# Kernel optimization log

Hardware: AMD Instinct MI355X
Metric: run time of the kernel (lower is better)

Reference implementation:

```python
import jax, jax.numpy as jnp
import numpy as np

H, NH, HD, KV, GS, L, F, V = 2048, 32, 64, 8, 4, 4, 8192, 32000
ROPE_BASE = 500000.0
EPS = 1e-5
WSCALE = 0.02


def setup_inputs() -> dict:
    key = jax.random.key(0)
    ks = jax.random.split(key, 12)
    B, S = 1, 2048
    return {
        "input_ids": jax.random.randint(ks[0], (B, S), 0, V),
        "embed": jax.random.normal(ks[1], (V, H), jnp.float32) * WSCALE,
        "ln1": jnp.ones((L, H), jnp.float32),
        "Wq": jax.random.normal(ks[2], (L, H, H), jnp.float32) * WSCALE,
        "Wk": jax.random.normal(ks[3], (L, KV * HD, H), jnp.float32) * WSCALE,
        "Wv": jax.random.normal(ks[4], (L, KV * HD, H), jnp.float32) * WSCALE,
        "Wo": jax.random.normal(ks[5], (L, H, H), jnp.float32) * WSCALE,
        "ln2": jnp.ones((L, H), jnp.float32),
        "Wg": jax.random.normal(ks[6], (L, F, H), jnp.float32) * WSCALE,
        "Wu": jax.random.normal(ks[7], (L, F, H), jnp.float32) * WSCALE,
        "Wd": jax.random.normal(ks[8], (L, H, F), jnp.float32) * WSCALE,
        "final_ln": jnp.ones((H,), jnp.float32),
    }


def _rms_norm(x, w):
    return x * jax.lax.rsqrt(jnp.mean(x * x, axis=-1, keepdims=True) + EPS) * w


def reference(input_ids, embed, ln1, Wq, Wk, Wv, Wo, ln2, Wg, Wu, Wd, final_ln):
    B, S = input_ids.shape
    h = embed[input_ids]                                   # [B,S,H]

    # RoPE tables (position_offset=0, prompt phase)
    dim_half = HD // 2
    inv_freq = 1.0 / (ROPE_BASE ** (jnp.arange(dim_half, dtype=jnp.float32) / dim_half))
    ang = jnp.arange(S, dtype=jnp.float32)[:, None] * inv_freq  # [S,dim_half]
    sin = jnp.sin(ang)[None, :, None, :]
    cos = jnp.cos(ang)[None, :, None, :]

    def rope(x):  # x: [B,S,heads,HD], halves layout as in source
        xe, xo = x[..., :dim_half], x[..., dim_half:2 * dim_half]
        return jnp.concatenate([xe * cos - xo * sin, xo * cos + xe * sin], axis=-1)

    causal = jnp.triu(jnp.ones((S, S), bool), k=1)          # [S,S]
    scale = 1.0 / (HD ** 0.5)

    for i in range(L):
        hn = _rms_norm(h, ln1[i])
        q = (hn @ Wq[i].T).reshape(B, S, NH, HD)
        k = (hn @ Wk[i].T).reshape(B, S, KV, HD)
        v = (hn @ Wv[i].T).reshape(B, S, KV, HD)
        q, k = rope(q), rope(k)
        ke = jnp.repeat(k, GS, axis=2)                      # GQA expand -> [B,S,NH,HD]
        ve = jnp.repeat(v, GS, axis=2)
        scores = jnp.einsum('bqhd,bkhd->bhqk', q, ke) * scale
        scores = jnp.where(causal[None, None], -jnp.inf, scores)
        attn = jax.nn.softmax(scores, axis=-1)
        out = jnp.einsum('bhqk,bkhd->bqhd', attn, ve).reshape(B, S, H)
        h = h + out @ Wo[i].T
        hn = _rms_norm(h, ln2[i])
        h = h + (jax.nn.silu(hn @ Wg[i].T) * (hn @ Wu[i].T)) @ Wd[i].T

    h = _rms_norm(h, final_ln)
    logits = h @ embed.T                                    # tied lm_head
    return logits
```

## Files before the change

### kernel.cpp

```cpp
#include <hip/hip_runtime.h>
#include <math.h>

#define HDIM 2048
#define SEQ 2048
#define NHEADS 32
#define KVH 8
#define HEADD 64
#define FDIM 8192
#define NLAYERS 4
#define VOCAB 32000

typedef __attribute__((ext_vector_type(4))) float f32x4;
typedef __attribute__((ext_vector_type(8))) short bf16x8;

__device__ __forceinline__ unsigned short f2b(float f) {
    unsigned int u = __float_as_uint(f);
    u += 0x7fff + ((u >> 16) & 1);
    return (unsigned short)(u >> 16);
}

__device__ __forceinline__ int xcd_swz(int bid, int nwg) {
    int xcd = bid & 7, lin = bid >> 3;
    int q = nwg >> 3, r = nwg & 7;
    return (xcd < r ? xcd * (q + 1) : r * (q + 1) + (xcd - r) * q) + lin;
}

#define GLL(gp, lp) __builtin_amdgcn_global_load_lds( \
    (const __attribute__((address_space(1))) void*)(gp), \
    (__attribute__((address_space(3))) void*)(lp), 16, 0, 0)

__device__ __forceinline__ void bar() {
    asm volatile("" ::: "memory");
    __builtin_amdgcn_s_barrier();
    asm volatile("" ::: "memory");
}

__global__ __launch_bounds__(256) void k_f2b(const float* __restrict__ src,
                                             unsigned short* __restrict__ dst, long n) {
    const long stride = (long)gridDim.x * 256 * 8;
    for (long i = ((long)blockIdx.x * 256 + threadIdx.x) * 8; i < n; i += stride) {
        float4 a = *(const float4*)(src + i);
        float4 b = *(const float4*)(src + i + 4);
        alignas(16) unsigned short t[8] = {f2b(a.x), f2b(a.y), f2b(a.z), f2b(a.w),
                                           f2b(b.x), f2b(b.y), f2b(b.z), f2b(b.w)};
        *(uint4*)(dst + i) = *(const uint4*)t;
    }
}

__global__ __launch_bounds__(256) void k_f2b_qkv(const float* __restrict__ Wq,
                                                 const float* __restrict__ Wk,
                                                 const float* __restrict__ Wv,
                                                 unsigned short* __restrict__ dst) {
    const long total = (long)NLAYERS * 3072 * 256;
    const long stride = (long)gridDim.x * 256;
    for (long u = (long)blockIdx.x * 256 + threadIdx.x; u < total; u += stride) {
        long l = u / (3072 * 256);
        long rem = u - l * (3072 * 256);
        long row = rem >> 8, cv = rem & 255;
        const float* src;
        if (row < 2048)      src = Wq + ((l * 2048 + row) << 11) + (cv << 3);
        else if (row < 2560) src = Wk + ((l * 512 + row - 2048) << 11) + (cv << 3);
        else                 src = Wv + ((l * 512 + row - 2560) << 11) + (cv << 3);
        float4 a = *(const float4*)src;
        float4 b = *(const float4*)(src + 4);
        alignas(16) unsigned short t[8] = {f2b(a.x), f2b(a.y), f2b(a.z), f2b(a.w),
                                           f2b(b.x), f2b(b.y), f2b(b.z), f2b(b.w)};
        *(uint4*)(dst + (u << 3)) = *(const uint4*)t;
    }
}

__global__ __launch_bounds__(256) void k_f2b_gu(const float* __restrict__ Wg,
                                                const float* __restrict__ Wu,
                                                unsigned short* __restrict__ dst) {
    const long total = (long)NLAYERS * 16384 * 256;
    const long stride = (long)gridDim.x * 256;
    for (long u = (long)blockIdx.x * 256 + threadIdx.x; u < total; u += stride) {
        long l = u / (16384 * 256);
        long rem = u - l * (16384 * 256);
        long row = rem >> 8, cv = rem & 255;
        long f = row >> 1;
        const float* src = ((row & 1) ? Wu : Wg) + ((l * FDIM + f) << 11) + (cv << 3);
        float4 a = *(const float4*)src;
        float4 b = *(const float4*)(src + 4);
        alignas(16) unsigned short t[8] = {f2b(a.x), f2b(a.y), f2b(a.z), f2b(a.w),
                                           f2b(b.x), f2b(b.y), f2b(b.z), f2b(b.w)};
        *(uint4*)(dst + (u << 3)) = *(const uint4*)t;
    }
}

template <int MODE, int K, int LDA, int LDB>
__global__ __launch_bounds__(512) void k_gemm256(const unsigned short* __restrict__ A,
                                                 const unsigned short* __restrict__ B,
                                                 float* __restrict__ C,
                                                 unsigned short* __restrict__ Cg,
                                                 int ldc, int mtiles, int nt,
                                                 long cstride) {
    constexpr int nK = K / 64;
    static_assert(nK >= 4 && (nK & 1) == 0, "nK must be even >= 4");
    __shared__ unsigned short As[2][2][128 * 64];
    __shared__ unsigned short Bs[2][2][128 * 64];
    const int tid  = threadIdx.x;
    const int lane = tid & 63;
    const int w    = tid >> 6;
    const int wm   = w >> 2, wn = w & 3;
    const int swz  = xcd_swz(blockIdx.x, gridDim.x);
    const int kslice = swz / nt;
    const int tile   = swz - kslice * nt;
    const int bm   = (tile % mtiles) * 256, bn = (tile / mtiles) * 256;
    const int r16  = lane & 15;
    const int l4   = lane >> 4;
    const int sw   = r16 & 7;

    const int srow = lane >> 3;
    const int scol = ((lane & 7) ^ srow) * 8;
    const unsigned short* Abase = A + (size_t)kslice * K
                                + (size_t)(bm + w * 16 + srow) * LDA + scol;
    const unsigned short* Bbase = B + (size_t)kslice * K
                                + (size_t)(bn + w * 16 + srow) * LDB + scol;

#define STG_A(bb, hh, kk) do { \
    GLL(Abase + (size_t)(hh) * 128 * LDA + (kk),       &As[(bb)][(hh)][(w * 16) * 64]); \
    GLL(Abase + (size_t)((hh) * 128 + 8) * LDA + (kk), &As[(bb)][(hh)][(w * 16 + 8) * 64]); \
} while (0)
#define STG_B(bb, hh, kk) do { \
    GLL(Bbase + (size_t)(hh) * 128 * LDB + (kk),       &Bs[(bb)][(hh)][(w * 16) * 64]); \
    GLL(Bbase + (size_t)((hh) * 128 + 8) * LDB + (kk), &Bs[(bb)][(hh)][(w * 16 + 8) * 64]); \
} while (0)

    f32x4 acc[8][4] = {};
    const int cb0 = ((0 + l4) ^ sw) * 8;
    const int cb1 = ((4 + l4) ^ sw) * 8;

    STG_A(0, 0, 0); STG_A(0, 1, 0); STG_B(0, 0, 0); STG_B(0, 1, 0);
    STG_B(1, 0, 64); STG_B(1, 1, 64); STG_A(1, 0, 64);
    asm volatile("s_waitcnt vmcnt(6)" ::: "memory");
    bar();

#define BLOAD(b) do { \
    const unsigned short* _Bh = Bs[b][wn >> 1]; \
    _Pragma("unroll") \
    for (int _n = 0; _n < 4; _n++) { \
        bq[_n][0] = *(const bf16x8*)&_Bh[((wn & 1) * 64 + _n * 16 + r16) * 64 + cb0]; \
        bq[_n][1] = *(const bf16x8*)&_Bh[((wn & 1) * 64 + _n * 16 + r16) * 64 + cb1]; \
    } \
} while (0)

#define PHASE(b, p, EXTRA, TAIL) do { \
    constexpr int _m0 = 2 * (p), _m1 = _m0 + 1; \
    const unsigned short* _Ah = As[b][_m0 >> 2]; \
    bf16x8 _a00 = *(const bf16x8*)&_Ah[(wm * 16 + (_m0 & 3) * 32 + r16) * 64 + cb0]; \
    bf16x8 _a01 = *(const bf16x8*)&_Ah[(wm * 16 + (_m0 & 3) * 32 + r16) * 64 + cb1]; \
    bf16x8 _a10 = *(const bf16x8*)&_Ah[(wm * 16 + (_m1 & 3) * 32 + r16) * 64 + cb0]; \
    bf16x8 _a11 = *(const bf16x8*)&_Ah[(wm * 16 + (_m1 & 3) * 32 + r16) * 64 + cb1]; \
    EXTRA; \
    bar(); \
    asm volatile("s_waitcnt lgkmcnt(0)" ::: "memory"); \
    __builtin_amdgcn_sched_barrier(0); \
    __builtin_amdgcn_s_setprio(1); \
    _Pragma("unroll") \
    for (int _n = 0; _n < 4; _n++) { \
        acc[_m0][_n] = __builtin_amdgcn_mfma_f32_16x16x32_bf16(_a00, bq[_n][0], acc[_m0][_n], 0, 0, 0); \
        acc[_m0][_n] = __builtin_amdgcn_mfma_f32_16x16x32_bf16(_a01, bq[_n][1], acc[_m0][_n], 0, 0, 0); \
    } \
    _Pragma("unroll") \
    for (int _n = 0; _n < 4; _n++) { \
        acc[_m1][_n] = __builtin_amdgcn_mfma_f32_16x16x32_bf16(_a10, bq[_n][0], acc[_m1][_n], 0, 0, 0); \
        acc[_m1][_n] = __builtin_amdgcn_mfma_f32_16x16x32_bf16(_a11, bq[_n][1], acc[_m1][_n], 0, 0, 0); \
    } \
    __builtin_amdgcn_s_setprio(0); \
    TAIL; \
    bar(); \
} while (0)

#define TILE_STEADY(b, t) do { \
    bf16x8 bq[4][2]; \
    PHASE(b, 0, { BLOAD(b); STG_A((b) ^ 1, 1, ((t) + 1) * 64); }, ); \
    PHASE(b, 1, STG_B(b, 0, ((t) + 2) * 64), ); \
    PHASE(b, 2, STG_B(b, 1, ((t) + 2) * 64), ); \
    PHASE(b, 3, STG_A(b, 0, ((t) + 2) * 64), \
          asm volatile("s_waitcnt vmcnt(6)" ::: "memory")); \
} while (0)

#define TILE_2NDLAST(b, t) do { \
    bf16x8 bq[4][2]; \
    PHASE(b, 0, { BLOAD(b); STG_A((b) ^ 1, 1, ((t) + 1) * 64); }, ); \
    PHASE(b, 1, , ); \
    PHASE(b, 2, , ); \
    PHASE(b, 3, , asm volatile("s_waitcnt vmcnt(0)" ::: "memory")); \
} while (0)

#define TILE_LAST(b) do { \
    bf16x8 bq[4][2]; \
    PHASE(b, 0, BLOAD(b), ); \
    PHASE(b, 1, , ); \
    PHASE(b, 2, , ); \
    PHASE(b, 3, , ); \
} while (0)

    for (int t = 0; t < nK - 2; t += 2) {
        TILE_STEADY(0, t);
        TILE_STEADY(1, t + 1);
    }
    TILE_2NDLAST(0, nK - 2);
    TILE_LAST(1);

#undef TILE_STEADY
#undef TILE_2NDLAST
#undef TILE_LAST
#undef PHASE
#undef BLOAD
#undef STG_A
#undef STG_B

    if (MODE == 0) C += (size_t)kslice * cstride;
    const int r0 = l4 * 4;
#pragma unroll
    for (int m = 0; m < 8; m++)
#pragma unroll
        for (int n = 0; n < 4; n++)
#pragma unroll
            for (int j = 0; j < 4; j++) {
                int row = bm + wm * 16 + m * 32 + r0 + j;
                int col = bn + wn * 64 + n * 16 + r16;
                if (MODE == 0) {
                    C[(size_t)row * ldc + col] = acc[m][n][j];
                } else {
                    float v0 = acc[m][n][j];
                    float v1 = __shfl_xor(v0, 1, 64);
                    if (!(r16 & 1)) {
                        float val = v0 / (1.f + __expf(-v0)) * v1;
                        Cg[(size_t)row * ldc + (col >> 1)] = f2b(val);
                    }
                }
            }
}

__global__ __launch_bounds__(256) void k_radd4(float* __restrict__ h,
                                               const float* __restrict__ P, long n4) {
    const long n = n4 * 4;
    const long stride = (long)gridDim.x * 256;
    for (long i = (long)blockIdx.x * 256 + threadIdx.x; i < n4; i += stride) {
        float4 a = ((const float4*)P)[i];
        float4 b = ((const float4*)(P + n))[i];
        float4 c = ((const float4*)(P + 2 * n))[i];
        float4 d = ((const float4*)(P + 3 * n))[i];
        float4 hh = ((float4*)h)[i];
        hh.x += a.x + b.x + c.x + d.x;
        hh.y += a.y + b.y + c.y + d.y;
        hh.z += a.z + b.z + c.z + d.z;
        hh.w += a.w + b.w + c.w + d.w;
        ((float4*)h)[i] = hh;
    }
}

template <bool ACCUM>
__global__ __launch_bounds__(256) void k_gemm_bf(const unsigned short* __restrict__ A,
                                                 const unsigned short* __restrict__ B,
                                                 float* __restrict__ C,
                                                 int K, int lda, int ldb, int ldc,
                                                 int mtiles) {
    __shared__ unsigned short As[128 * 32];
    __shared__ unsigned short Bs[128 * 32];
    const int tid  = threadIdx.x;
    const int lane = tid & 63;
    const int w    = tid >> 6;
    const int wm   = w >> 1, wn = w & 1;
    const int bid  = xcd_swz(blockIdx.x, gridDim.x);
    const int bm   = (bid % mtiles) * 128, bn = (bid / mtiles) * 128;
    const int r16  = lane & 15;
    const int l4   = lane >> 4;

    const unsigned short* Ag = A + (size_t)(bm + w * 32 + (lane >> 2)) * lda + (lane & 3) * 8;
    const unsigned short* Bg = B + (size_t)(bn + w * 32 + (lane >> 2)) * ldb + (lane & 3) * 8;
    unsigned short* Al = As + w * 1024;
    unsigned short* Bl = Bs + w * 1024;

    f32x4 acc[4][4] = {};

    for (int k0 = 0; k0 < K; k0 += 32) {
        GLL(Ag + k0,                    Al);
        GLL(Ag + k0 + (size_t)16 * lda, Al + 512);
        GLL(Bg + k0,                    Bl);
        GLL(Bg + k0 + (size_t)16 * ldb, Bl + 512);
        __syncthreads();

        bf16x8 af[4], bf[4];
#pragma unroll
        for (int m = 0; m < 4; m++) af[m] = *(const bf16x8*)&As[(wm * 64 + m * 16 + r16) * 32 + l4 * 8];
#pragma unroll
        for (int n = 0; n < 4; n++) bf[n] = *(const bf16x8*)&Bs[(wn * 64 + n * 16 + r16) * 32 + l4 * 8];
#pragma unroll
        for (int m = 0; m < 4; m++)
#pragma unroll
            for (int n = 0; n < 4; n++)
                acc[m][n] = __builtin_amdgcn_mfma_f32_16x16x32_bf16(af[m], bf[n], acc[m][n], 0, 0, 0);
        __syncthreads();
    }

    const int r0 = l4 * 4;
#pragma unroll
    for (int m = 0; m < 4; m++)
#pragma unroll
        for (int n = 0; n < 4; n++)
#pragma unroll
            for (int j = 0; j < 4; j++) {
                int row = bm + wm * 64 + m * 16 + r0 + j;
                int col = bn + wn * 64 + n * 16 + r16;
                size_t idx = (size_t)row * ldc + col;
                if (ACCUM) C[idx] += acc[m][n][j];
                else       C[idx] = acc[m][n][j];
            }
}

template <bool ACCUM>
__global__ __launch_bounds__(256) void k_gemm(const float* __restrict__ A,
                                              const float* __restrict__ B,
                                              float* __restrict__ C,
                                              int K, int lda, int ldb, int ldc) {
    __shared__ unsigned short As[128][40];
    __shared__ unsigned short Bs[128][40];
    const int tid  = threadIdx.x;
    const int lane = tid & 63;
    const int wid  = tid >> 6;
    const int wm   = wid >> 1, wn = wid & 1;
    const int bm   = blockIdx.y * 128, bn = blockIdx.x * 128;
    const int arow = tid >> 1, ahalf = tid & 1;
    const float* Ab = A + (size_t)(bm + arow) * lda + ahalf * 16;
    const float* Bb = B + (size_t)(bn + arow) * ldb + ahalf * 16;
    const int r16 = lane & 15;
    const int kk  = (lane >> 4) * 8;

    f32x4 acc[4][4] = {};

    for (int k0 = 0; k0 < K; k0 += 32) {
        alignas(16) unsigned short ta[16], tb[16];
#pragma unroll
        for (int i = 0; i < 4; i++) {
            float4 av = *(const float4*)(Ab + k0 + i * 4);
            float4 bv = *(const float4*)(Bb + k0 + i * 4);
            ta[i*4+0] = f2b(av.x); ta[i*4+1] = f2b(av.y);
            ta[i*4+2] = f2b(av.z); ta[i*4+3] = f2b(av.w);
            tb[i*4+0] = f2b(bv.x); tb[i*4+1] = f2b(bv.y);
            tb[i*4+2] = f2b(bv.z); tb[i*4+3] = f2b(bv.w);
        }
        __syncthreads();
        *(uint4*)&As[arow][ahalf*16]     = *(const uint4*)&ta[0];
        *(uint4*)&As[arow][ahalf*16 + 8] = *(const uint4*)&ta[8];
        *(uint4*)&Bs[arow][ahalf*16]     = *(const uint4*)&tb[0];
        *(uint4*)&Bs[arow][ahalf*16 + 8] = *(const uint4*)&tb[8];
        __syncthreads();

        bf16x8 af[4], bf[4];
#pragma unroll
        for (int m = 0; m < 4; m++) af[m] = *(const bf16x8*)&As[wm*64 + m*16 + r16][kk];
#pragma unroll
        for (int n = 0; n < 4; n++) bf[n] = *(const bf16x8*)&Bs[wn*64 + n*16 + r16][kk];
#pragma unroll
        for (int m = 0; m < 4; m++)
#pragma unroll
            for (int n = 0; n < 4; n++)
                acc[m][n] = __builtin_amdgcn_mfma_f32_16x16x32_bf16(af[m], bf[n], acc[m][n], 0, 0, 0);
    }

    const int r0 = (lane >> 4) * 4;
#pragma unroll
    for (int m = 0; m < 4; m++)
#pragma unroll
        for (int n = 0; n < 4; n++)
#pragma unroll
            for (int j = 0; j < 4; j++) {
                int row = bm + wm*64 + m*16 + r0 + j;
                int col = bn + wn*64 + n*16 + r16;
                size_t idx = (size_t)row * ldc + col;
                if (ACCUM) C[idx] += acc[m][n][j];
                else       C[idx] = acc[m][n][j];
            }
}

__global__ __launch_bounds__(256) void k_gather(const int* __restrict__ ids,
                                                const float* __restrict__ embed,
                                                float* __restrict__ h) {
    const int s = blockIdx.x, tid = threadIdx.x;
    const int row = ids[s];
    const float4* src = (const float4*)(embed + (size_t)row * HDIM);
    float4* dst = (float4*)(h + (size_t)s * HDIM);
    dst[tid]       = src[tid];
    dst[tid + 256] = src[tid + 256];
}

__device__ __forceinline__ float rms_scale(float4 a, float4 b, int tid) {
    float sum = a.x*a.x + a.y*a.y + a.z*a.z + a.w*a.w
              + b.x*b.x + b.y*b.y + b.z*b.z + b.w*b.w;
#pragma unroll
    for (int off = 32; off; off >>= 1) sum += __shfl_xor(sum, off, 64);
    __shared__ float red[4];
    if ((tid & 63) == 0) red[tid >> 6] = sum;
    __syncthreads();
    float tot = red[0] + red[1] + red[2] + red[3];
    return rsqrtf(tot * (1.0f / HDIM) + 1e-5f);
}

__global__ __launch_bounds__(256) void k_rmsnorm_bf(unsigned short* __restrict__ out,
                                                    const float* __restrict__ in,
                                                    const float* __restrict__ w) {
    const int s = blockIdx.x, tid = threadIdx.x;
    const float4* x = (const float4*)(in + (size_t)s * HDIM);
    float4 a = x[tid*2], b = x[tid*2+1];
    float r = rms_scale(a, b, tid);
    const float4* wv = (const float4*)w;
    float4 wa = wv[tid*2], wb = wv[tid*2+1];
    alignas(16) unsigned short t[8];
    t[0] = f2b(a.x*r*wa.x); t[1] = f2b(a.y*r*wa.y);
    t[2] = f2b(a.z*r*wa.z); t[3] = f2b(a.w*r*wa.w);
    t[4] = f2b(b.x*r*wb.x); t[5] = f2b(b.y*r*wb.y);
    t[6] = f2b(b.z*r*wb.z); t[7] = f2b(b.w*r*wb.w);
    *(uint4*)(out + (size_t)s * HDIM + tid * 8) = *(const uint4*)t;
}

__global__ __launch_bounds__(256) void k_rmsnorm_f32(float* __restrict__ out,
                                                     const float* __restrict__ in,
                                                     const float* __restrict__ w) {
    const int s = blockIdx.x, tid = threadIdx.x;
    const float4* x = (const float4*)(in + (size_t)s * HDIM);
    float4 a = x[tid*2], b = x[tid*2+1];
    float r = rms_scale(a, b, tid);
    const float4* wv = (const float4*)w;
    float4 wa = wv[tid*2], wb = wv[tid*2+1];
    float4* o = (float4*)(out + (size_t)s * HDIM);
    float4 oa, ob;
    oa.x = a.x*r*wa.x; oa.y = a.y*r*wa.y; oa.z = a.z*r*wa.z; oa.w = a.w*r*wa.w;
    ob.x = b.x*r*wb.x; ob.y = b.y*r*wb.y; ob.z = b.z*r*wb.z; ob.w = b.w*r*wb.w;
    o[tid*2] = oa; o[tid*2+1] = ob;
}

template <bool TWO>
__global__ __launch_bounds__(256) void k_ropeq(const float* __restrict__ P0,
                                               const float* __restrict__ P1,
                                               unsigned short* __restrict__ q_bf) {
    const int s = blockIdx.x, tid = threadIdx.x;
    for (int idx = tid; idx < 1024; idx += 256) {
        int hh = idx >> 5, j = idx & 31;
        float invf = exp2f(-(float)j * (18.931568569324174f / 32.0f));
        float ang = (float)s * invf;
        float sn, cs;
        __sincosf(ang, &sn, &cs);
        size_t off = (size_t)s * 3072 + hh * 64 + j;
        float xe = P0[off]      + (TWO ? P1[off]      : 0.f);
        float xo = P0[off + 32] + (TWO ? P1[off + 32] : 0.f);
        unsigned short* o = q_bf + (size_t)s * HDIM + hh * 64 + j;
        o[0]  = f2b((xe * cs - xo * sn) * 0.125f);
        o[32] = f2b((xo * cs + xe * sn) * 0.125f);
    }
}

template <bool TWO>
__global__ __launch_bounds__(256) void k_prep_kv(const float* __restrict__ P0,
                                                 const float* __restrict__ P1,
                                                 unsigned short* __restrict__ kbf,
                                                 unsigned short* __restrict__ vtb) {
    const int s0 = blockIdx.x * 64, tid = threadIdx.x;
    for (int i = tid; i < 64 * 256; i += 256) {
        int r = i >> 8, idx = i & 255;
        int kvh = idx >> 5, j = idx & 31;
        int s = s0 + r;
        float invf = exp2f(-(float)j * (18.931568569324174f / 32.0f));
        float ang = (float)s * invf;
        float sn, cs;
        __sincosf(ang, &sn, &cs);
        size_t off = (size_t)s * 3072 + 2048 + kvh * 64 + j;
        float xe = P0[off]      + (TWO ? P1[off]      : 0.f);
        float xo = P0[off + 32] + (TWO ? P1[off + 32] : 0.f);
        unsigned short* o = kbf + ((size_t)kvh * SEQ + s) * 64 + j;
        o[0]  = f2b(xe * cs - xo * sn);
        o[32] = f2b(xo * cs + xe * sn);
    }
    __shared__ float Ls[64][65];
    for (int kvh = 0; kvh < KVH; kvh++) {
        __syncthreads();
        {
            int r = tid >> 2, c0 = (tid & 3) * 16;
            size_t off = (size_t)(s0 + r) * 3072 + 2560 + kvh * 64 + c0;
#pragma unroll
            for (int i = 0; i < 16; i += 4) {
                float4 x = *(const float4*)(P0 + off + i);
                if (TWO) {
                    float4 y = *(const float4*)(P1 + off + i);
                    x.x += y.x; x.y += y.y; x.z += y.z; x.w += y.w;
                }
                Ls[r][c0+i] = x.x; Ls[r][c0+i+1] = x.y;
                Ls[r][c0+i+2] = x.z; Ls[r][c0+i+3] = x.w;
            }
        }
        __syncthreads();
        {
            int d = tid >> 2, k0 = (tid & 3) * 16;
            alignas(16) unsigned short tmp[16];
#pragma unroll
            for (int i = 0; i < 16; i++) tmp[i] = f2b(Ls[k0 + i][d]);
            unsigned short* dst = vtb + ((size_t)kvh * 64 + d) * SEQ + s0 + k0;
            *(uint4*)dst       = *(const uint4*)tmp;
            *(uint4*)(dst + 8) = *(const uint4*)(tmp + 8);
        }
    }
}

__global__ __launch_bounds__(256) void k_attn2(const unsigned short* __restrict__ q_bf,
                                               const unsigned short* __restrict__ kbf,
                                               const unsigned short* __restrict__ vtb,
                                               unsigned short* __restrict__ aob) {
    const int hh  = blockIdx.y;
    const int qt  = gridDim.x - 1 - blockIdx.x;
    const int qb  = qt * 64;
    const int kvh = hh >> 2;
    const int tid = threadIdx.x, w = tid >> 6, lane = tid & 63;
    const int r16 = lane & 15;
    const int l4  = lane >> 4;

    __shared__ unsigned short Ks[64][72];
    __shared__ unsigned short Vs[64][72];
    __shared__ unsigned short Ps[64][72];

    bf16x8 qf[2];
    {
        const unsigned short* qrow = q_bf + (size_t)(qb + w*16 + r16) * HDIM + hh * 64;
        qf[0] = *(const bf16x8*)(qrow + l4 * 8);
        qf[1] = *(const bf16x8*)(qrow + 32 + l4 * 8);
    }

    float m[4] = {-1e30f, -1e30f, -1e30f, -1e30f};
    float l[4] = {0.f, 0.f, 0.f, 0.f};
    f32x4 out[4] = {};

    for (int t = 0; t <= qt; t++) {
        __syncthreads();
        {
            int r = tid >> 2, c0 = (tid & 3) * 16;
            const unsigned short* ksrc = kbf + ((size_t)kvh * SEQ + t*64 + r) * 64 + c0;
            *(uint4*)&Ks[r][c0]     = *(const uint4*)ksrc;
            *(uint4*)&Ks[r][c0 + 8] = *(const uint4*)(ksrc + 8);
            const unsigned short* vsrc = vtb + ((size_t)kvh * 64 + r) * SEQ + t*64 + c0;
            *(uint4*)&Vs[r][c0]     = *(const uint4*)vsrc;
            *(uint4*)&Vs[r][c0 + 8] = *(const uint4*)(vsrc + 8);
        }
        __syncthreads();

        f32x4 s[4] = {};
#pragma unroll
        for (int ks = 0; ks < 2; ks++)
#pragma unroll
            for (int n = 0; n < 4; n++) {
                bf16x8 kf = *(const bf16x8*)&Ks[n*16 + r16][ks*32 + l4*8];
                s[n] = __builtin_amdgcn_mfma_f32_16x16x32_bf16(qf[ks], kf, s[n], 0, 0, 0);
            }

        if (t == qt) {
#pragma unroll
            for (int n = 0; n < 4; n++)
#pragma unroll
                for (int j = 0; j < 4; j++) {
                    int qrow = w*16 + l4*4 + j;
                    int key  = n*16 + r16;
                    if (key > qrow) s[n][j] = -1e30f;
                }
        }

        float corr[4];
#pragma unroll
        for (int j = 0; j < 4; j++) {
            float mx = fmaxf(fmaxf(s[0][j], s[1][j]), fmaxf(s[2][j], s[3][j]));
#pragma unroll
            for (int off = 1; off < 16; off <<= 1) mx = fmaxf(mx, __shfl_xor(mx, off, 64));
            float mn = fmaxf(m[j], mx);
            corr[j] = __expf(m[j] - mn);
            m[j] = mn;
            float rs = 0.f;
#pragma unroll
            for (int n = 0; n < 4; n++) {
                float p = __expf(s[n][j] - mn);
                s[n][j] = p;
                rs += p;
            }
#pragma unroll
            for (int off = 1; off < 16; off <<= 1) rs += __shfl_xor(rs, off, 64);
            l[j] = l[j] * corr[j] + rs;
        }

#pragma unroll
        for (int n = 0; n < 4; n++)
#pragma unroll
            for (int j = 0; j < 4; j++)
                Ps[w*16 + l4*4 + j][n*16 + r16] = f2b(s[n][j]);

#pragma unroll
        for (int n = 0; n < 4; n++)
#pragma unroll
            for (int j = 0; j < 4; j++) out[n][j] *= corr[j];

#pragma unroll
        for (int ks = 0; ks < 2; ks++) {
            bf16x8 pa = *(const bf16x8*)&Ps[w*16 + r16][ks*32 + l4*8];
#pragma unroll
            for (int n = 0; n < 4; n++) {
                bf16x8 vf = *(const bf16x8*)&Vs[n*16 + r16][ks*32 + l4*8];
                out[n] = __builtin_amdgcn_mfma_f32_16x16x32_bf16(pa, vf, out[n], 0, 0, 0);
            }
        }
    }

#pragma unroll
    for (int n = 0; n < 4; n++)
#pragma unroll
        for (int j = 0; j < 4; j++) {
            int row = qb + w*16 + l4*4 + j;
            int col = hh*64 + n*16 + r16;
            aob[(size_t)row * HDIM + col] = f2b(out[n][j] / l[j]);
        }
}

__global__ __launch_bounds__(256) void k_rope(float* __restrict__ x, int nh,
                                              float scale, int ld) {
    const int s = blockIdx.x, tid = threadIdx.x;
    const int total = nh * 32;
    for (int idx = tid; idx < total; idx += 256) {
        int hh = idx >> 5, j = idx & 31;
        float invf = exp2f(-(float)j * (18.931568569324174f / 32.0f));
        float ang = (float)s * invf;
        float sn, cs;
        __sincosf(ang, &sn, &cs);
        float* p = x + (size_t)s * ld + hh * 64 + j;
        float xe = p[0], xo = p[32];
        p[0]  = (xe * cs - xo * sn) * scale;
        p[32] = (xo * cs + xe * sn) * scale;
    }
}

__global__ __launch_bounds__(256) void k_vtrans(const float* __restrict__ v, int ldv,
                                                unsigned short* __restrict__ vt) {
    __shared__ float Ls[64][65];
    const int tid = threadIdx.x;
    const int kb = blockIdx.x * 64, db = blockIdx.y * 64;
    {
        int r = tid >> 2, c0 = (tid & 3) * 16;
        const float* src = v + (size_t)(kb + r) * ldv + db + c0;
#pragma unroll
        for (int i = 0; i < 16; i += 4) {
            float4 x = *(const float4*)(src + i);
            Ls[r][c0+i] = x.x; Ls[r][c0+i+1] = x.y;
            Ls[r][c0+i+2] = x.z; Ls[r][c0+i+3] = x.w;
        }
    }
    __syncthreads();
    {
        int d = tid >> 2, k0 = (tid & 3) * 16;
        alignas(16) unsigned short tmp[16];
#pragma unroll
        for (int i = 0; i < 16; i++) tmp[i] = f2b(Ls[k0 + i][d]);
        unsigned short* dst = vt + (size_t)(db + d) * SEQ + kb + k0;
        *(uint4*)dst       = *(const uint4*)tmp;
        *(uint4*)(dst + 8) = *(const uint4*)(tmp + 8);
    }
}

__global__ __launch_bounds__(256) void k_attn_f32(float* __restrict__ q, int ldq,
                                                  const float* __restrict__ kb, int ldk,
                                                  const unsigned short* __restrict__ vt) {
    const int hh  = blockIdx.y;
    const int qt  = gridDim.x - 1 - blockIdx.x;
    const int qb  = qt * 64;
    const int kvh = hh >> 2;
    const int tid = threadIdx.x, w = tid >> 6, lane = tid & 63;
    const int r16 = lane & 15;
    const int l4  = lane >> 4;

    __shared__ unsigned short Ks[64][72];
    __shared__ unsigned short Vs[64][72];
    __shared__ unsigned short Ps[64][72];

    bf16x8 qf[2];
    {
        const float* qrow = q + (size_t)(qb + w*16 + r16) * ldq + hh * 64;
#pragma unroll
        for (int ks = 0; ks < 2; ks++) {
            alignas(16) unsigned short t[8];
#pragma unroll
            for (int i = 0; i < 8; i += 4) {
                float4 x = *(const float4*)(qrow + ks*32 + l4*8 + i);
                t[i] = f2b(x.x); t[i+1] = f2b(x.y); t[i+2] = f2b(x.z); t[i+3] = f2b(x.w);
            }
            qf[ks] = *(const bf16x8*)t;
        }
    }

    float m[4] = {-1e30f, -1e30f, -1e30f, -1e30f};
    float l[4] = {0.f, 0.f, 0.f, 0.f};
    f32x4 out[4] = {};

    for (int t = 0; t <= qt; t++) {
        __syncthreads();
        {
            int r = tid >> 2, c0 = (tid & 3) * 16;
            const float* src = kb + (size_t)(t*64 + r) * ldk + kvh*64 + c0;
            alignas(16) unsigned short tmp[16];
#pragma unroll
            for (int i = 0; i < 16; i += 4) {
                float4 x = *(const float4*)(src + i);
                tmp[i]   = f2b(x.x); tmp[i+1] = f2b(x.y);
                tmp[i+2] = f2b(x.z); tmp[i+3] = f2b(x.w);
            }
            *(uint4*)&Ks[r][c0]     = *(const uint4*)tmp;
            *(uint4*)&Ks[r][c0 + 8] = *(const uint4*)(tmp + 8);
            const unsigned short* vsrc = vt + (size_t)(kvh*64 + r) * SEQ + t*64 + c0;
            *(uint4*)&Vs[r][c0]     = *(const uint4*)vsrc;
            *(uint4*)&Vs[r][c0 + 8] = *(const uint4*)(vsrc + 8);
        }
        __syncthreads();

        f32x4 s[4] = {};
#pragma unroll
        for (int ks = 0; ks < 2; ks++)
#pragma unroll
            for (int n = 0; n < 4; n++) {
                bf16x8 kf = *(const bf16x8*)&Ks[n*16 + r16][ks*32 + l4*8];
                s[n] = __builtin_amdgcn_mfma_f32_16x16x32_bf16(qf[ks], kf, s[n], 0, 0, 0);
            }

        if (t == qt) {
#pragma unroll
            for (int n = 0; n < 4; n++)
#pragma unroll
                for (int j = 0; j < 4; j++) {
                    int qrow = w*16 + l4*4 + j;
                    int key  = n*16 + r16;
                    if (key > qrow) s[n][j] = -1e30f;
                }
        }

        float corr[4];
#pragma unroll
        for (int j = 0; j < 4; j++) {
            float mx = fmaxf(fmaxf(s[0][j], s[1][j]), fmaxf(s[2][j], s[3][j]));
#pragma unroll
            for (int off = 1; off < 16; off <<= 1) mx = fmaxf(mx, __shfl_xor(mx, off, 64));
            float mn = fmaxf(m[j], mx);
            corr[j] = __expf(m[j] - mn);
            m[j] = mn;
            float rs = 0.f;
#pragma unroll
            for (int n = 0; n < 4; n++) {
                float p = __expf(s[n][j] - mn);
                s[n][j] = p;
                rs += p;
            }
#pragma unroll
            for (int off = 1; off < 16; off <<= 1) rs += __shfl_xor(rs, off, 64);
            l[j] = l[j] * corr[j] + rs;
        }

#pragma unroll
        for (int n = 0; n < 4; n++)
#pragma unroll
            for (int j = 0; j < 4; j++)
                Ps[w*16 + l4*4 + j][n*16 + r16] = f2b(s[n][j]);

#pragma unroll
        for (int n = 0; n < 4; n++)
#pragma unroll
            for (int j = 0; j < 4; j++) out[n][j] *= corr[j];

#pragma unroll
        for (int ks = 0; ks < 2; ks++) {
            bf16x8 pa = *(const bf16x8*)&Ps[w*16 + r16][ks*32 + l4*8];
#pragma unroll
            for (int n = 0; n < 4; n++) {
                bf16x8 vf = *(const bf16x8*)&Vs[n*16 + r16][ks*32 + l4*8];
                out[n] = __builtin_amdgcn_mfma_f32_16x16x32_bf16(pa, vf, out[n], 0, 0, 0);
            }
        }
    }

#pragma unroll
    for (int n = 0; n < 4; n++)
#pragma unroll
        for (int j = 0; j < 4; j++)
            q[(size_t)(qb + w*16 + l4*4 + j) * ldq + hh*64 + n*16 + r16] = out[n][j] / l[j];
}

__global__ __launch_bounds__(256) void k_silu(float* __restrict__ g,
                                              const float* __restrict__ u) {
    const size_t i = (size_t)blockIdx.x * 256 + threadIdx.x;
    float4 gv = ((const float4*)g)[i];
    float4 uv = ((const float4*)u)[i];
    gv.x = gv.x / (1.f + __expf(-gv.x)) * uv.x;
    gv.y = gv.y / (1.f + __expf(-gv.y)) * uv.y;
    gv.z = gv.z / (1.f + __expf(-gv.z)) * uv.z;
    gv.w = gv.w / (1.f + __expf(-gv.w)) * uv.w;
    ((float4*)g)[i] = gv;
}

extern "C" void kernel_launch(void* const* d_in, const int* in_sizes, int n_in,
                              void* d_out, int out_size, void* d_ws, size_t ws_size,
                              hipStream_t stream) {
    (void)in_sizes; (void)n_in; (void)out_size;
    const int*   ids   = (const int*)d_in[0];
    const float* embed = (const float*)d_in[1];
    const float* ln1   = (const float*)d_in[2];
    const float* Wq    = (const float*)d_in[3];
    const float* Wk    = (const float*)d_in[4];
    const float* Wv    = (const float*)d_in[5];
    const float* Wo    = (const float*)d_in[6];
    const float* ln2   = (const float*)d_in[7];
    const float* Wg    = (const float*)d_in[8];
    const float* Wu    = (const float*)d_in[9];
    const float* Wd    = (const float*)d_in[10];
    const float* fln   = (const float*)d_in[11];
    float* out = (float*)d_out;

    char* base = (char*)d_ws;
    size_t off = 0;
    auto alloc = [&](size_t bytes) -> char* {
        char* r = base + off;
        off = (off + bytes + 255) & ~(size_t)255;
        return r;
    };
    float* h     = (float*)alloc((size_t)SEQ * HDIM * 4);
    unsigned short* hn_bf = (unsigned short*)alloc((size_t)SEQ * HDIM * 2);
    unsigned short* aob   = (unsigned short*)alloc((size_t)SEQ * HDIM * 2);
    unsigned short* gated = (unsigned short*)alloc((size_t)SEQ * FDIM * 2);
    unsigned short* q_bf  = (unsigned short*)alloc((size_t)SEQ * HDIM * 2);
    unsigned short* kbf   = (unsigned short*)alloc((size_t)KVH * SEQ * 64 * 2);
    unsigned short* vtb   = (unsigned short*)alloc((size_t)KVH * 64 * SEQ * 2);
    unsigned short* wqkv  = (unsigned short*)alloc((size_t)NLAYERS * 3072 * HDIM * 2);
    unsigned short* wo_b  = (unsigned short*)alloc((size_t)NLAYERS * HDIM * HDIM * 2);
    unsigned short* wgu   = (unsigned short*)alloc((size_t)NLAYERS * 2 * FDIM * HDIM * 2);
    unsigned short* wd_b  = (unsigned short*)alloc((size_t)NLAYERS * HDIM * FDIM * 2);
    unsigned short* emb_b = (unsigned short*)alloc((size_t)VOCAB * HDIM * 2);
    char* Sreg = alloc((size_t)4 * SEQ * HDIM * 4);
    const size_t REQ_MAIN = off;
    const size_t REQ_FB2  = REQ_MAIN - (size_t)4 * SEQ * HDIM * 4
                          + (((size_t)SEQ * 3072 * 4 + 255) & ~(size_t)255);

    const long LQ = (long)HDIM * HDIM;
    const long LGU = 2L * FDIM * HDIM;
    const long LG = (long)FDIM * HDIM;
    const long MSZ = (long)SEQ * 3072;
    const long HSZ = (long)SEQ * HDIM;

    if (ws_size >= REQ_MAIN) {
        float* Pf = (float*)Sreg;
        k_f2b_qkv<<<2048, 256, 0, stream>>>(Wq, Wk, Wv, wqkv);
        k_f2b_gu<<<2048, 256, 0, stream>>>(Wg, Wu, wgu);
        k_f2b<<<2048, 256, 0, stream>>>(Wo, wo_b, (long)NLAYERS * LQ);
        k_f2b<<<2048, 256, 0, stream>>>(Wd, wd_b, (long)NLAYERS * LG);
        k_f2b<<<2048, 256, 0, stream>>>(embed, emb_b, (long)VOCAB * HDIM);

        k_gather<<<SEQ, 256, 0, stream>>>(ids, embed, h);

        for (int i = 0; i < NLAYERS; i++) {
            k_rmsnorm_bf<<<SEQ, 256, 0, stream>>>(hn_bf, h, ln1 + i * HDIM);
            k_gemm256<0, 1024, 2048, 2048><<<192, 512, 0, stream>>>(
                hn_bf, wqkv + (long)i * 3072 * HDIM, Pf, nullptr, 3072, 8, 96, MSZ);
            k_ropeq<true><<<SEQ, 256, 0, stream>>>(Pf, Pf + MSZ, q_bf);
            k_prep_kv<true><<<SEQ / 64, 256, 0, stream>>>(Pf, Pf + MSZ, kbf, vtb);
            k_attn2<<<dim3(SEQ / 64, NHEADS), 256, 0, stream>>>(q_bf, kbf, vtb, aob);
            k_gemm256<0, 512, 2048, 2048><<<256, 512, 0, stream>>>(
                aob, wo_b + (long)i * LQ, Pf, nullptr, 2048, 8, 64, HSZ);
            k_radd4<<<2048, 256, 0, stream>>>(h, Pf, HSZ / 4);
            k_rmsnorm_bf<<<SEQ, 256, 0, stream>>>(hn_bf, h, ln2 + i * HDIM);
            k_gemm256<2, 2048, 2048, 2048><<<512, 512, 0, stream>>>(
                hn_bf, wgu + (long)i * LGU, nullptr, gated, FDIM, 8, 512, 0);
            k_gemm256<0, 2048, 8192, 8192><<<256, 512, 0, stream>>>(
                gated, wd_b + (long)i * LG, Pf, nullptr, 2048, 8, 64, HSZ);
            k_radd4<<<2048, 256, 0, stream>>>(h, Pf, HSZ / 4);
        }

        k_rmsnorm_bf<<<SEQ, 256, 0, stream>>>(hn_bf, h, fln);
        k_gemm256<0, 2048, 2048, 2048><<<1000, 512, 0, stream>>>(
            hn_bf, emb_b, out, nullptr, VOCAB, 8, 1000, 0);
    } else if (ws_size >= REQ_FB2) {
        float* qkv = (float*)Sreg;
        k_f2b_qkv<<<2048, 256, 0, stream>>>(Wq, Wk, Wv, wqkv);
        k_f2b_gu<<<2048, 256, 0, stream>>>(Wg, Wu, wgu);
        k_f2b<<<2048, 256, 0, stream>>>(Wo, wo_b, (long)NLAYERS * LQ);
        k_f2b<<<2048, 256, 0, stream>>>(Wd, wd_b, (long)NLAYERS * LG);
        k_f2b<<<2048, 256, 0, stream>>>(embed, emb_b, (long)VOCAB * HDIM);

        k_gather<<<SEQ, 256, 0, stream>>>(ids, embed, h);

        for (int i = 0; i < NLAYERS; i++) {
            k_rmsnorm_bf<<<SEQ, 256, 0, stream>>>(hn_bf, h, ln1 + i * HDIM);
            k_gemm_bf<false><<<16 * 24, 256, 0, stream>>>(hn_bf, wqkv + (long)i*3072*HDIM,
                                                          qkv, HDIM, HDIM, HDIM, 3072, 16);
            k_ropeq<false><<<SEQ, 256, 0, stream>>>(qkv, nullptr, q_bf);
            k_prep_kv<false><<<SEQ / 64, 256, 0, stream>>>(qkv, nullptr, kbf, vtb);
            k_attn2<<<dim3(SEQ / 64, NHEADS), 256, 0, stream>>>(q_bf, kbf, vtb, aob);
            k_gemm_bf<true><<<16 * 16, 256, 0, stream>>>(aob, wo_b + (long)i*LQ, h,
                                                         HDIM, HDIM, HDIM, HDIM, 16);
            k_rmsnorm_bf<<<SEQ, 256, 0, stream>>>(hn_bf, h, ln2 + i * HDIM);
            k_gemm256<2, 2048, 2048, 2048><<<512, 512, 0, stream>>>(
                hn_bf, wgu + (long)i * LGU, nullptr, gated, FDIM, 8, 512, 0);
            k_gemm_bf<true><<<16 * 16, 256, 0, stream>>>(gated, wd_b + (long)i*LG, h,
                                                         FDIM, FDIM, FDIM, HDIM, 16);
        }

        k_rmsnorm_bf<<<SEQ, 256, 0, stream>>>(hn_bf, h, fln);
        k_gemm256<0, 2048, 2048, 2048><<<1000, 512, 0, stream>>>(
            hn_bf, emb_b, out, nullptr, VOCAB, 8, 1000, 0);
    } else {
        float* ws = (float*)d_ws;
        const size_t M4 = (size_t)4 * 1024 * 1024;
        const size_t M1 = (size_t)1 * 1024 * 1024;
        float* fh  = ws;
        float* hn  = fh + M4;
        float* q   = hn + M4;
        float* kb  = q  + M4;
        float* vb  = kb + M1;
        float* gb  = vb + M1;
        float* ub  = gb + M4;
        unsigned short* fvt = (unsigned short*)(ub + M4);

        k_gather<<<SEQ, 256, 0, stream>>>(ids, embed, fh);

        for (int i = 0; i < NLAYERS; i++) {
            const float* Wq_i = Wq + (size_t)i * HDIM * HDIM;
            const float* Wk_i = Wk + (size_t)i * 512 * HDIM;
            const float* Wv_i = Wv + (size_t)i * 512 * HDIM;
            const float* Wo_i = Wo + (size_t)i * HDIM * HDIM;
            const float* Wg_i = Wg + (size_t)i * FDIM * HDIM;
            const float* Wu_i = Wu + (size_t)i * FDIM * HDIM;
            const float* Wd_i = Wd + (size_t)i * HDIM * FDIM;

            k_rmsnorm_f32<<<SEQ, 256, 0, stream>>>(hn, fh, ln1 + i * HDIM);
            k_gemm<false><<<dim3(16, 16), 256, 0, stream>>>(hn, Wq_i, q,  HDIM, HDIM, HDIM, HDIM);
            k_gemm<false><<<dim3(4, 16),  256, 0, stream>>>(hn, Wk_i, kb, HDIM, HDIM, HDIM, 512);
            k_gemm<false><<<dim3(4, 16),  256, 0, stream>>>(hn, Wv_i, vb, HDIM, HDIM, HDIM, 512);
            k_rope<<<SEQ, 256, 0, stream>>>(q,  NHEADS, 0.125f, HDIM);
            k_rope<<<SEQ, 256, 0, stream>>>(kb, KVH,    1.0f,  512);
            k_vtrans<<<dim3(SEQ/64, 8), 256, 0, stream>>>(vb, 512, fvt);
            k_attn_f32<<<dim3(SEQ/64, NHEADS), 256, 0, stream>>>(q, HDIM, kb, 512, fvt);
            k_gemm<true><<<dim3(16, 16), 256, 0, stream>>>(q, Wo_i, fh, HDIM, HDIM, HDIM, HDIM);

            k_rmsnorm_f32<<<SEQ, 256, 0, stream>>>(hn, fh, ln2 + i * HDIM);
            for (int fc = 0; fc < 4; fc++) {
                const float* Wg_c = Wg_i + (size_t)fc * 2048 * HDIM;
                const float* Wu_c = Wu_i + (size_t)fc * 2048 * HDIM;
                const float* Wd_c = Wd_i + (size_t)fc * 2048;
                k_gemm<false><<<dim3(16, 16), 256, 0, stream>>>(hn, Wg_c, gb, HDIM, HDIM, HDIM, 2048);
                k_gemm<false><<<dim3(16, 16), 256, 0, stream>>>(hn, Wu_c, ub, HDIM, HDIM, HDIM, 2048);
                k_silu<<<4096, 256, 0, stream>>>(gb, ub);
                k_gemm<true><<<dim3(16, 16), 256, 0, stream>>>(gb, Wd_c, fh, 2048, 2048, FDIM, HDIM);
            }
        }

        k_rmsnorm_f32<<<SEQ, 256, 0, stream>>>(hn, fh, fln);
        k_gemm<false><<<dim3(VOCAB/128, 16), 256, 0, stream>>>(hn, embed, out, HDIM, HDIM, HDIM, VOCAB);
    }
}
```

Baseline: 2.429 ms.

## Fuse residual add with RMSNorm and process two KV tiles per attention iteration

Replaces the separate residual-add and RMSNorm kernels with one kernel that sums the four split-K partials into h, writes h back, and emits the normalized bf16 activations for the next GEMM, including the next layer's ln1 and the final norm. This removes launches and one full re-read of the hidden state per residual. The attention kernel now loads two K/V tiles into double-sized shared buffers per loop iteration and does one softmax rescale over both, halving barriers and rescale passes. The cost is more shared memory and register pressure in attention, which may reduce occupancy.

```diff
diff --git a/kernel.cpp b/kernel.cpp
--- a/kernel.cpp
+++ b/kernel.cpp
@@ -235,22 +235,78 @@
             }
 }
 
-__global__ __launch_bounds__(256) void k_radd4(float* __restrict__ h,
-                                               const float* __restrict__ P, long n4) {
-    const long n = n4 * 4;
-    const long stride = (long)gridDim.x * 256;
-    for (long i = (long)blockIdx.x * 256 + threadIdx.x; i < n4; i += stride) {
-        float4 a = ((const float4*)P)[i];
-        float4 b = ((const float4*)(P + n))[i];
-        float4 c = ((const float4*)(P + 2 * n))[i];
-        float4 d = ((const float4*)(P + 3 * n))[i];
-        float4 hh = ((float4*)h)[i];
-        hh.x += a.x + b.x + c.x + d.x;
-        hh.y += a.y + b.y + c.y + d.y;
-        hh.z += a.z + b.z + c.z + d.z;
-        hh.w += a.w + b.w + c.w + d.w;
-        ((float4*)h)[i] = hh;
-    }
+__device__ __forceinline__ float rms_scale(float4 a, float4 b, int tid) {
+    float sum = a.x*a.x + a.y*a.y + a.z*a.z + a.w*a.w
+              + b.x*b.x + b.y*b.y + b.z*b.z + b.w*b.w;
+#pragma unroll
+    for (int off = 32; off; off >>= 1) sum += __shfl_xor(sum, off, 64);
+    __shared__ float red[4];
+    if ((tid & 63) == 0) red[tid >> 6] = sum;
+    __syncthreads();
+    float tot = red[0] + red[1] + red[2] + red[3];
+    return rsqrtf(tot * (1.0f / HDIM) + 1e-5f);
+}
+
+__global__ __launch_bounds__(256) void k_rms_radd(unsigned short* __restrict__ out,
+                                                  float* __restrict__ h,
+                                                  const float* __restrict__ P, long n,
+                                                  const float* __restrict__ w) {
+    const int s = blockIdx.x, tid = threadIdx.x;
+    const size_t base = (size_t)s * HDIM + tid * 8;
+    float4 a = *(const float4*)(h + base);
+    float4 b = *(const float4*)(h + base + 4);
+#pragma unroll
+    for (int k = 0; k < 4; k++) {
+        const float* p = P + (size_t)k * n + base;
+        float4 x = *(const float4*)p;
+        float4 y = *(const float4*)(p + 4);
+        a.x += x.x; a.y += x.y; a.z += x.z; a.w += x.w;
+        b.x += y.x; b.y += y.y; b.z += y.z; b.w += y.w;
+    }
+    *(float4*)(h + base) = a;
+    *(float4*)(h + base + 4) = b;
+    float r = rms_scale(a, b, tid);
+    const float4* wv = (const float4*)w;
+    float4 wa = wv[tid*2], wb = wv[tid*2+1];
+    alignas(16) unsigned short t[8];
+    t[0] = f2b(a.x*r*wa.x); t[1] = f2b(a.y*r*wa.y);
+    t[2] = f2b(a.z*r*wa.z); t[3] = f2b(a.w*r*wa.w);
+    t[4] = f2b(b.x*r*wb.x); t[5] = f2b(b.y*r*wb.y);
+    t[6] = f2b(b.z*r*wb.z); t[7] = f2b(b.w*r*wb.w);
+    *(uint4*)(out + base) = *(const uint4*)t;
+}
+
+__global__ __launch_bounds__(256) void k_rmsnorm_bf(unsigned short* __restrict__ out,
+                                                    const float* __restrict__ in,
+                                                    const float* __restrict__ w) {
+    const int s = blockIdx.x, tid = threadIdx.x;
+    const float4* x = (const float4*)(in + (size_t)s * HDIM);
+    float4 a = x[tid*2], b = x[tid*2+1];
+    float r = rms_scale(a, b, tid);
+    const float4* wv = (const float4*)w;
+    float4 wa = wv[tid*2], wb = wv[tid*2+1];
+    alignas(16) unsigned short t[8];
+    t[0] = f2b(a.x*r*wa.x); t[1] = f2b(a.y*r*wa.y);
+    t[2] = f2b(a.z*r*wa.z); t[3] = f2b(a.w*r*wa.w);
+    t[4] = f2b(b.x*r*wb.x); t[5] = f2b(b.y*r*wb.y);
+    t[6] = f2b(b.z*r*wb.z); t[7] = f2b(b.w*r*wb.w);
+    *(uint4*)(out + (size_t)s * HDIM + tid * 8) = *(const uint4*)t;
+}
+
+__global__ __launch_bounds__(256) void k_rmsnorm_f32(float* __restrict__ out,
+                                                     const float* __restrict__ in,
+                                                     const float* __restrict__ w) {
+    const int s = blockIdx.x, tid = threadIdx.x;
+    const float4* x = (const float4*)(in + (size_t)s * HDIM);
+    float4 a = x[tid*2], b = x[tid*2+1];
+    float r = rms_scale(a, b, tid);
+    const float4* wv = (const float4*)w;
+    float4 wa = wv[tid*2], wb = wv[tid*2+1];
+    float4* o = (float4*)(out + (size_t)s * HDIM);
+    float4 oa, ob;
+    oa.x = a.x*r*wa.x; oa.y = a.y*r*wa.y; oa.z = a.z*r*wa.z; oa.w = a.w*r*wa.w;
+    ob.x = b.x*r*wb.x; ob.y = b.y*r*wb.y; ob.z = b.z*r*wb.z; ob.w = b.w*r*wb.w;
+    o[tid*2] = oa; o[tid*2+1] = ob;
 }
 
 template <bool ACCUM>
@@ -386,51 +442,6 @@
     float4* dst = (float4*)(h + (size_t)s * HDIM);
     dst[tid]       = src[tid];
     dst[tid + 256] = src[tid + 256];
-}
-
-__device__ __forceinline__ float rms_scale(float4 a, float4 b, int tid) {
-    float sum = a.x*a.x + a.y*a.y + a.z*a.z + a.w*a.w
-              + b.x*b.x + b.y*b.y + b.z*b.z + b.w*b.w;
-#pragma unroll
-    for (int off = 32; off; off >>= 1) sum += __shfl_xor(sum, off, 64);
-    __shared__ float red[4];
-    if ((tid & 63) == 0) red[tid >> 6] = sum;
-    __syncthreads();
-    float tot = red[0] + red[1] + red[2] + red[3];
-    return rsqrtf(tot * (1.0f / HDIM) + 1e-5f);
-}
-
-__global__ __launch_bounds__(256) void k_rmsnorm_bf(unsigned short* __restrict__ out,
-                                                    const float* __restrict__ in,
-                                                    const float* __restrict__ w) {
-    const int s = blockIdx.x, tid = threadIdx.x;
-    const float4* x = (const float4*)(in + (size_t)s * HDIM);
-    float4 a = x[tid*2], b = x[tid*2+1];
-    float r = rms_scale(a, b, tid);
-    const float4* wv = (const float4*)w;
-    float4 wa = wv[tid*2], wb = wv[tid*2+1];
-    alignas(16) unsigned short t[8];
-    t[0] = f2b(a.x*r*wa.x); t[1] = f2b(a.y*r*wa.y);
-    t[2] = f2b(a.z*r*wa.z); t[3] = f2b(a.w*r*wa.w);
-    t[4] = f2b(b.x*r*wb.x); t[5] = f2b(b.y*r*wb.y);
-    t[6] = f2b(b.z*r*wb.z); t[7] = f2b(b.w*r*wb.w);
-    *(uint4*)(out + (size_t)s * HDIM + tid * 8) = *(const uint4*)t;
-}
-
-__global__ __launch_bounds__(256) void k_rmsnorm_f32(float* __restrict__ out,
-                                                     const float* __restrict__ in,
-                                                     const float* __restrict__ w) {
-    const int s = blockIdx.x, tid = threadIdx.x;
-    const float4* x = (const float4*)(in + (size_t)s * HDIM);
-    float4 a = x[tid*2], b = x[tid*2+1];
-    float r = rms_scale(a, b, tid);
-    const float4* wv = (const float4*)w;
-    float4 wa = wv[tid*2], wb = wv[tid*2+1];
-    float4* o = (float4*)(out + (size_t)s * HDIM);
-    float4 oa, ob;
-    oa.x = a.x*r*wa.x; oa.y = a.y*r*wa.y; oa.z = a.z*r*wa.z; oa.w = a.w*r*wa.w;
-    ob.x = b.x*r*wb.x; ob.y = b.y*r*wb.y; ob.z = b.z*r*wb.z; ob.w = b.w*r*wb.w;
-    o[tid*2] = oa; o[tid*2+1] = ob;
 }
 
 template <bool TWO>
@@ -516,8 +527,8 @@
     const int r16 = lane & 15;
     const int l4  = lane >> 4;
 
-    __shared__ unsigned short Ks[64][72];
-    __shared__ unsigned short Vs[64][72];
+    __shared__ unsigned short Ks[2][64][72];
+    __shared__ unsigned short Vs[2][64][72];
     __shared__ unsigned short Ps[64][72];
 
     bf16x8 qf[2];
@@ -530,44 +541,67 @@
     float m[4] = {-1e30f, -1e30f, -1e30f, -1e30f};
     float l[4] = {0.f, 0.f, 0.f, 0.f};
     f32x4 out[4] = {};
-
-    for (int t = 0; t <= qt; t++) {
+    const int ntiles = qt + 1;
+
+    for (int t0 = 0; t0 < ntiles; t0 += 2) {
+        const bool two = (t0 + 1 < ntiles);
         __syncthreads();
         {
             int r = tid >> 2, c0 = (tid & 3) * 16;
-            const unsigned short* ksrc = kbf + ((size_t)kvh * SEQ + t*64 + r) * 64 + c0;
-            *(uint4*)&Ks[r][c0]     = *(const uint4*)ksrc;
-            *(uint4*)&Ks[r][c0 + 8] = *(const uint4*)(ksrc + 8);
-            const unsigned short* vsrc = vtb + ((size_t)kvh * 64 + r) * SEQ + t*64 + c0;
-            *(uint4*)&Vs[r][c0]     = *(const uint4*)vsrc;
-            *(uint4*)&Vs[r][c0 + 8] = *(const uint4*)(vsrc + 8);
+            const unsigned short* ks0 = kbf + ((size_t)kvh * SEQ + t0*64 + r) * 64 + c0;
+            *(uint4*)&Ks[0][r][c0]     = *(const uint4*)ks0;
+            *(uint4*)&Ks[0][r][c0 + 8] = *(const uint4*)(ks0 + 8);
+            const unsigned short* vs0 = vtb + ((size_t)kvh * 64 + r) * SEQ + t0*64 + c0;
+            *(uint4*)&Vs[0][r][c0]     = *(const uint4*)vs0;
+            *(uint4*)&Vs[0][r][c0 + 8] = *(const uint4*)(vs0 + 8);
+            if (two) {
+                const unsigned short* ks1 = ks0 + 64 * 64;
+                *(uint4*)&Ks[1][r][c0]     = *(const uint4*)ks1;
+                *(uint4*)&Ks[1][r][c0 + 8] = *(const uint4*)(ks1 + 8);
+                const unsigned short* vs1 = vs0 + 64;
+                *(uint4*)&Vs[1][r][c0]     = *(const uint4*)vs1;
+                *(uint4*)&Vs[1][r][c0 + 8] = *(const uint4*)(vs1 + 8);
+            }
         }
         __syncthreads();
 
-        f32x4 s[4] = {};
+        f32x4 s[2][4] = {};
 #pragma unroll
         for (int ks = 0; ks < 2; ks++)
 #pragma unroll
             for (int n = 0; n < 4; n++) {
-                bf16x8 kf = *(const bf16x8*)&Ks[n*16 + r16][ks*32 + l4*8];
-                s[n] = __builtin_amdgcn_mfma_f32_16x16x32_bf16(qf[ks], kf, s[n], 0, 0, 0);
-            }
-
-        if (t == qt) {
+                bf16x8 kf = *(const bf16x8*)&Ks[0][n*16 + r16][ks*32 + l4*8];
+                s[0][n] = __builtin_amdgcn_mfma_f32_16x16x32_bf16(qf[ks], kf, s[0][n], 0, 0, 0);
+            }
+        if (two) {
+#pragma unroll
+            for (int ks = 0; ks < 2; ks++)
+#pragma unroll
+                for (int n = 0; n < 4; n++) {
+                    bf16x8 kf = *(const bf16x8*)&Ks[1][n*16 + r16][ks*32 + l4*8];
+                    s[1][n] = __builtin_amdgcn_mfma_f32_16x16x32_bf16(qf[ks], kf, s[1][n], 0, 0, 0);
+                }
+        }
+
+        const int dh = qt - t0;
+        if (dh < 2) {
 #pragma unroll
             for (int n = 0; n < 4; n++)
 #pragma unroll
                 for (int j = 0; j < 4; j++) {
                     int qrow = w*16 + l4*4 + j;
                     int key  = n*16 + r16;
-                    if (key > qrow) s[n][j] = -1e30f;
+                    if (key > qrow) { if (dh == 0) s[0][n][j] = -1e30f; else s[1][n][j] = -1e30f; }
                 }
         }
 
         float corr[4];
 #pragma unroll
         for (int j = 0; j < 4; j++) {
-            float mx = fmaxf(fmaxf(s[0][j], s[1][j]), fmaxf(s[2][j], s[3][j]));
+            float mx = fmaxf(fmaxf(s[0][0][j], s[0][1][j]), fmaxf(s[0][2][j], s[0][3][j]));
+            if (two)
+                mx = fmaxf(mx, fmaxf(fmaxf(s[1][0][j], s[1][1][j]),
+                                     fmaxf(s[1][2][j], s[1][3][j])));
 #pragma unroll
             for (int off = 1; off < 16; off <<= 1) mx = fmaxf(mx, __shfl_xor(mx, off, 64));
             float mn = fmaxf(m[j], mx);
@@ -576,9 +610,17 @@
             float rs = 0.f;
 #pragma unroll
             for (int n = 0; n < 4; n++) {
-                float p = __expf(s[n][j] - mn);
-                s[n][j] = p;
+                float p = __expf(s[0][n][j] - mn);
+                s[0][n][j] = p;
                 rs += p;
+            }
+            if (two) {
+#pragma unroll
+                for (int n = 0; n < 4; n++) {
+                    float p = __expf(s[1][n][j] - mn);
+                    s[1][n][j] = p;
+                    rs += p;
+                }
             }
 #pragma unroll
             for (int off = 1; off < 16; off <<= 1) rs += __shfl_xor(rs, off, 64);
@@ -588,21 +630,36 @@
 #pragma unroll
         for (int n = 0; n < 4; n++)
 #pragma unroll
+            for (int j = 0; j < 4; j++) out[n][j] *= corr[j];
+
+#pragma unroll
+        for (int n = 0; n < 4; n++)
+#pragma unroll
             for (int j = 0; j < 4; j++)
-                Ps[w*16 + l4*4 + j][n*16 + r16] = f2b(s[n][j]);
-
-#pragma unroll
-        for (int n = 0; n < 4; n++)
-#pragma unroll
-            for (int j = 0; j < 4; j++) out[n][j] *= corr[j];
-
+                Ps[w*16 + l4*4 + j][n*16 + r16] = f2b(s[0][n][j]);
 #pragma unroll
         for (int ks = 0; ks < 2; ks++) {
             bf16x8 pa = *(const bf16x8*)&Ps[w*16 + r16][ks*32 + l4*8];
 #pragma unroll
             for (int n = 0; n < 4; n++) {
-                bf16x8 vf = *(const bf16x8*)&Vs[n*16 + r16][ks*32 + l4*8];
+                bf16x8 vf = *(const bf16x8*)&Vs[0][n*16 + r16][ks*32 + l4*8];
                 out[n] = __builtin_amdgcn_mfma_f32_16x16x32_bf16(pa, vf, out[n], 0, 0, 0);
+            }
+        }
+        if (two) {
+#pragma unroll
+            for (int n = 0; n < 4; n++)
+#pragma unroll
+                for (int j = 0; j < 4; j++)
+                    Ps[w*16 + l4*4 + j][n*16 + r16] = f2b(s[1][n][j]);
+#pragma unroll
+            for (int ks = 0; ks < 2; ks++) {
+                bf16x8 pa = *(const bf16x8*)&Ps[w*16 + r16][ks*32 + l4*8];
+#pragma unroll
+                for (int n = 0; n < 4; n++) {
+                    bf16x8 vf = *(const bf16x8*)&Vs[1][n*16 + r16][ks*32 + l4*8];
+                    out[n] = __builtin_amdgcn_mfma_f32_16x16x32_bf16(pa, vf, out[n], 0, 0, 0);
+                }
             }
         }
     }
@@ -854,9 +911,9 @@
         k_f2b<<<2048, 256, 0, stream>>>(embed, emb_b, (long)VOCAB * HDIM);
 
         k_gather<<<SEQ, 256, 0, stream>>>(ids, embed, h);
+        k_rmsnorm_bf<<<SEQ, 256, 0, stream>>>(hn_bf, h, ln1);
 
         for (int i = 0; i < NLAYERS; i++) {
-            k_rmsnorm_bf<<<SEQ, 256, 0, stream>>>(hn_bf, h, ln1 + i * HDIM);
             k_gemm256<0, 1024, 2048, 2048><<<192, 512, 0, stream>>>(
                 hn_bf, wqkv + (long)i * 3072 * HDIM, Pf, nullptr, 3072, 8, 96, MSZ);
             k_ropeq<true><<<SEQ, 256, 0, stream>>>(Pf, Pf + MSZ, q_bf);
@@ -864,16 +921,15 @@
             k_attn2<<<dim3(SEQ / 64, NHEADS), 256, 0, stream>>>(q_bf, kbf, vtb, aob);
             k_gemm256<0, 512, 2048, 2048><<<256, 512, 0, stream>>>(
                 aob, wo_b + (long)i * LQ, Pf, nullptr, 2048, 8, 64, HSZ);
-            k_radd4<<<2048, 256, 0, stream>>>(h, Pf, HSZ / 4);
-            k_rmsnorm_bf<<<SEQ, 256, 0, stream>>>(hn_bf, h, ln2 + i * HDIM);
+            k_rms_radd<<<SEQ, 256, 0, stream>>>(hn_bf, h, Pf, HSZ, ln2 + i * HDIM);
             k_gemm256<2, 2048, 2048, 2048><<<512, 512, 0, stream>>>(
                 hn_bf, wgu + (long)i * LGU, nullptr, gated, FDIM, 8, 512, 0);
             k_gemm256<0, 2048, 8192, 8192><<<256, 512, 0, stream>>>(
                 gated, wd_b + (long)i * LG, Pf, nullptr, 2048, 8, 64, HSZ);
-            k_radd4<<<2048, 256, 0, stream>>>(h, Pf, HSZ / 4);
-        }
-
-        k_rmsnorm_bf<<<SEQ, 256, 0, stream>>>(hn_bf, h, fln);
+            const float* nw = (i + 1 < NLAYERS) ? ln1 + (i + 1) * HDIM : fln;
+            k_rms_radd<<<SEQ, 256, 0, stream>>>(hn_bf, h, Pf, HSZ, nw);
+        }
+
         k_gemm256<0, 2048, 2048, 2048><<<1000, 512, 0, stream>>>(
             hn_bf, emb_b, out, nullptr, VOCAB, 8, 1000, 0);
     } else if (ws_size >= REQ_FB2) {
```

Result: no change. 2.411 ms (-0.7%).
